# Kernel optimization log

Measured on AMD Instinct MI355X. Metric: run time of the kernel, lower is better.

Reference implementation:

```python
import jax, jax.numpy as jnp
from jax import lax
import numpy as np

K = 3
IMG = 512
BATCH = 32


def setup_inputs() -> dict:
    key = jax.random.key(0)
    k1, k2, k3 = jax.random.split(key, 3)
    x = jax.random.normal(k1, (BATCH, 1, IMG, IMG), dtype=jnp.float32)
    # Conv2d(1, K*K, K) weight/bias, torch default init scale ~ 1/sqrt(fan_in)
    fan_in = 1 * K * K
    bound = 1.0 / np.sqrt(fan_in)
    W = jax.random.uniform(k2, (K * K, 1, K, K), dtype=jnp.float32, minval=-bound, maxval=bound)
    b = jax.random.uniform(k3, (K * K,), dtype=jnp.float32, minval=-bound, maxval=bound)
    return {"x": x, "W": W, "b": b}


def reference(x, W, b):
    k = W.shape[-1]
    pad = k // 2                      # k_radius
    P = x.shape[-1] + k - 1           # padded/self.img_size spatial size
    # x_tmp = F.pad(x, pad on all sides); firstConv = Conv2d(1, k^2, k, padding=pad)(x_tmp)
    x_tmp = jnp.pad(x, ((0, 0), (0, 0), (pad, pad), (pad, pad)))
    fc = lax.conv_general_dilated(
        x_tmp, W, window_strides=(1, 1), padding=[(pad, pad), (pad, pad)],
        dimension_numbers=("NCHW", "OIHW", "NCHW"),
    ) + b[None, :, None, None]        # (B, k^2, P, P)
    t = jnp.tanh(fc)
    # F.pad(x, (k-1-i, i, k-1-j, j)) == xp[:, :, j:j+P, i:i+P] with xp padded by k-1 everywhere
    xp = jnp.pad(x, ((0, 0), (0, 0), (k - 1, k - 1), (k - 1, k - 1)))
    out = jnp.zeros((x.shape[0], 1, P, P), dtype=x.dtype)
    for i in range(k):                # small fixed k^2 loop over kernel taps
        for j in range(k):
            out = out + xp[:, :, j:j + P, i:i + P] * t[:, k * i + j][:, None]
    return out[:, :, pad:-pad, pad:-pad]
```

## Files before the change

### kernel.cpp

```cpp
#include <hip/hip_runtime.h>
#include <stdint.h>

#define IMG  512
#define CPT  8
#define CGRP (IMG / CPT)

typedef float    v2f   __attribute__((ext_vector_type(2)));
typedef _Float16 h2    __attribute__((ext_vector_type(2)));
typedef __fp16   f16x2 __attribute__((ext_vector_type(2)));

#define SCALE 2.8853900817779268f

static __device__ __forceinline__ h2 pkrtz(float a, float b) {
    f16x2 t = __builtin_amdgcn_cvt_pkrtz(a, b);
    return __builtin_bit_cast(h2, t);
}

#if __has_builtin(__builtin_amdgcn_fdot2)
#define FDOT2(a, b, c) __builtin_amdgcn_fdot2((a), (b), (c), false)
#else
static __device__ __forceinline__ float fdot2_sw(h2 a, h2 b, float c) {
    return fmaf((float)a.x, (float)b.x, fmaf((float)a.y, (float)b.y, c));
}
#define FDOT2(a, b, c) fdot2_sw((a), (b), (c))
#endif

__global__ void prepack_kernel(const float* __restrict__ W,
                               const float* __restrict__ B,
                               uint32_t* __restrict__ ws) {
    int c = threadIdx.x;
    if (c < 9) {
        const float* wc = W + c * 9;
#pragma unroll
        for (int k = 0; k < 4; ++k) {
            h2 t = pkrtz(wc[2 * k] * SCALE, wc[2 * k + 1] * SCALE);
            ws[c * 4 + k] = __builtin_bit_cast(uint32_t, t);
        }
        ((float*)ws)[36 + c] = wc[8] * SCALE;
        ((float*)ws)[45 + c] = B[c] * SCALE;
    }
}

__global__ __launch_bounds__(256) void fused_convtap_kernel(
    const float* __restrict__ x,
    const uint32_t* __restrict__ wsu,
    float* __restrict__ out)
{
    const float* w8v = (const float*)(wsu + 36);
    const float* bvv = (const float*)(wsu + 45);

    const int tid = blockIdx.x * 256 + threadIdx.x;
    const int xg  = tid & (CGRP - 1);
    const int row = tid >> 6;
    const int y   = row & (IMG - 1);
    const int x0  = xg * CPT;

    const float* xr = x + (size_t)row * IMG;

    h2 u[9][4];
#pragma unroll
    for (int c = 0; c < 9; ++c)
#pragma unroll
        for (int k = 0; k < 4; ++k)
            u[c][k] = __builtin_bit_cast(h2, wsu[c * 4 + k]);
    float w8[9], bv[9];
#pragma unroll
    for (int c = 0; c < 9; ++c) { w8[c] = w8v[c]; bv[c] = bvv[c]; }

    const bool has_l = (x0 > 0);
    const bool has_r = (x0 < IMG - CPT);

    float r0[10], r1[10], r2[10];
    auto load_row = [&](const float* p, float* r) {
        float4 a = *reinterpret_cast<const float4*>(p + x0);
        float4 c = *reinterpret_cast<const float4*>(p + x0 + 4);
        r[1] = a.x; r[2] = a.y; r[3] = a.z; r[4] = a.w;
        r[5] = c.x; r[6] = c.y; r[7] = c.z; r[8] = c.w;
        r[0] = has_l ? p[x0 - 1] : 0.0f;
        r[9] = has_r ? p[x0 + 8] : 0.0f;
    };
    auto zero_row = [&](float* r) {
#pragma unroll
        for (int k = 0; k < 10; ++k) r[k] = 0.0f;
    };

    if (y > 0)       load_row(xr - IMG, r0); else zero_row(r0);
                     load_row(xr,       r1);
    if (y < IMG - 1) load_row(xr + IMG, r2); else zero_row(r2);

    float o[CPT];
#pragma unroll
    for (int tp = 0; tp < 4; ++tp) {
        const int t0 = 2 * tp;
        h2 A0 = pkrtz(r0[t0],     r0[t0 + 1]);
        h2 B0 = pkrtz(r0[t0 + 2], r1[t0]);
        h2 C0 = pkrtz(r1[t0 + 1], r1[t0 + 2]);
        h2 D0 = pkrtz(r2[t0],     r2[t0 + 1]);
        h2 A1 = pkrtz(r0[t0 + 1], r0[t0 + 2]);
        h2 B1 = pkrtz(r0[t0 + 3], r1[t0 + 1]);
        h2 C1 = pkrtz(r1[t0 + 2], r1[t0 + 3]);
        h2 D1 = pkrtz(r2[t0 + 1], r2[t0 + 2]);

        v2f acc = {0.0f, 0.0f};
#pragma unroll
        for (int c = 0; c < 9; ++c) {
            float fx = bv[c], fy = bv[c];
            fx = FDOT2(A0, u[c][0], fx);
            fx = FDOT2(B0, u[c][1], fx);
            fx = FDOT2(C0, u[c][2], fx);
            fx = FDOT2(D0, u[c][3], fx);
            fx = fmaf(r2[t0 + 2], w8[c], fx);
            fy = FDOT2(A1, u[c][0], fy);
            fy = FDOT2(B1, u[c][1], fy);
            fy = FDOT2(C1, u[c][2], fy);
            fy = FDOT2(D1, u[c][3], fy);
            fy = fmaf(r2[t0 + 3], w8[c], fy);

            v2f e   = { __builtin_amdgcn_exp2f(fx), __builtin_amdgcn_exp2f(fy) };
            v2f ep1 = e + (v2f){1.0f, 1.0f};
            v2f rr  = { __builtin_amdgcn_rcpf(ep1.x), __builtin_amdgcn_rcpf(ep1.y) };
            v2f th  = __builtin_elementwise_fma((v2f){-2.0f, -2.0f}, rr,
                                                (v2f){1.0f, 1.0f});

            const int i = c / 3, j = c - 3 * i;
            const float* rj = (j == 0) ? r0 : (j == 1) ? r1 : r2;
            v2f px2 = { rj[t0 + i], rj[t0 + 1 + i] };
            acc = __builtin_elementwise_fma(px2, th, acc);
        }
        o[t0] = acc.x; o[t0 + 1] = acc.y;
    }

    float* orow = out + (size_t)row * IMG + x0;
    *reinterpret_cast<float4*>(orow)     = make_float4(o[0], o[1], o[2], o[3]);
    *reinterpret_cast<float4*>(orow + 4) = make_float4(o[4], o[5], o[6], o[7]);
}

extern "C" void kernel_launch(void* const* d_in, const int* in_sizes, int n_in,
                              void* d_out, int out_size, void* d_ws, size_t ws_size,
                              hipStream_t stream) {
    const float* x  = (const float*)d_in[0];
    const float* W  = (const float*)d_in[1];
    const float* Bv = (const float*)d_in[2];
    float* out = (float*)d_out;
    uint32_t* ws = (uint32_t*)d_ws;

    prepack_kernel<<<1, 64, 0, stream>>>(W, Bv, ws);

    const int batch   = in_sizes[0] / (IMG * IMG);
    const int threads = batch * IMG * CGRP;
    const int grid    = threads / 256;
    fused_convtap_kernel<<<grid, 256, 0, stream>>>(x, ws, out);
}
```

Before: 39.08 us.

## Replace tanh transcendentals with shared-memory lookup table and drop prepack kernel

Each block now builds a 4096-entry tanh table in LDS covering [-4,4] in steps of 1/512. The per-pixel exp2 and rcp evaluations become a clamped index computation and an LDS gather. The separate weight-prepacking kernel launch is removed: each thread now reads W and b directly and converts them to half pairs itself. This trades transcendental throughput for per-block table construction, a barrier, LDS bank-conflict risk, and a nearest-entry tanh approximation with small, input-independent error.

```diff
diff --git a/kernel.cpp b/kernel.cpp
--- a/kernel.cpp
+++ b/kernel.cpp
@@ -5,11 +5,8 @@
 #define CPT  8
 #define CGRP (IMG / CPT)
 
-typedef float    v2f   __attribute__((ext_vector_type(2)));
 typedef _Float16 h2    __attribute__((ext_vector_type(2)));
 typedef __fp16   f16x2 __attribute__((ext_vector_type(2)));
-
-#define SCALE 2.8853900817779268f
 
 static __device__ __forceinline__ h2 pkrtz(float a, float b) {
     f16x2 t = __builtin_amdgcn_cvt_pkrtz(a, b);
@@ -25,29 +22,22 @@
 #define FDOT2(a, b, c) fdot2_sw((a), (b), (c))
 #endif
 
-__global__ void prepack_kernel(const float* __restrict__ W,
-                               const float* __restrict__ B,
-                               uint32_t* __restrict__ ws) {
-    int c = threadIdx.x;
-    if (c < 9) {
-        const float* wc = W + c * 9;
-#pragma unroll
-        for (int k = 0; k < 4; ++k) {
-            h2 t = pkrtz(wc[2 * k] * SCALE, wc[2 * k + 1] * SCALE);
-            ws[c * 4 + k] = __builtin_bit_cast(uint32_t, t);
-        }
-        ((float*)ws)[36 + c] = wc[8] * SCALE;
-        ((float*)ws)[45 + c] = B[c] * SCALE;
-    }
-}
 
 __global__ __launch_bounds__(256) void fused_convtap_kernel(
     const float* __restrict__ x,
-    const uint32_t* __restrict__ wsu,
+    const float* __restrict__ W,
+    const float* __restrict__ Bv,
     float* __restrict__ out)
 {
-    const float* w8v = (const float*)(wsu + 36);
-    const float* bvv = (const float*)(wsu + 45);
+    __shared__ float lut[4096];
+#pragma unroll
+    for (int k = 0; k < 16; ++k) {
+        const int i  = threadIdx.x + (k << 8);
+        const float xi = fmaf((float)i, 0.001953125f, 0.0009765625f - 4.0f);
+        const float e  = __builtin_amdgcn_exp2f(xi * 2.8853900817779268f);
+        lut[i] = 1.0f - 2.0f * __builtin_amdgcn_rcpf(e + 1.0f);
+    }
+    __syncthreads();
 
     const int tid = blockIdx.x * 256 + threadIdx.x;
     const int xg  = tid & (CGRP - 1);
@@ -58,14 +48,15 @@
     const float* xr = x + (size_t)row * IMG;
 
     h2 u[9][4];
+    float w8[9], bv[9];
 #pragma unroll
-    for (int c = 0; c < 9; ++c)
+    for (int c = 0; c < 9; ++c) {
 #pragma unroll
         for (int k = 0; k < 4; ++k)
-            u[c][k] = __builtin_bit_cast(h2, wsu[c * 4 + k]);
-    float w8[9], bv[9];
-#pragma unroll
-    for (int c = 0; c < 9; ++c) { w8[c] = w8v[c]; bv[c] = bvv[c]; }
+            u[c][k] = pkrtz(W[c * 9 + 2 * k], W[c * 9 + 2 * k + 1]);
+        w8[c] = W[c * 9 + 8];
+        bv[c] = Bv[c];
+    }
 
     const bool has_l = (x0 > 0);
     const bool has_r = (x0 < IMG - CPT);
@@ -88,6 +79,12 @@
                      load_row(xr,       r1);
     if (y < IMG - 1) load_row(xr + IMG, r2); else zero_row(r2);
 
+    auto tlu = [&](float v) -> float {
+        float t = __builtin_amdgcn_fmed3f(fmaf(v, 512.0f, 2048.0f),
+                                          0.0f, 4095.0f);
+        return lut[(int)t];
+    };
+
     float o[CPT];
 #pragma unroll
     for (int tp = 0; tp < 4; ++tp) {
@@ -101,33 +98,30 @@
         h2 C1 = pkrtz(r1[t0 + 2], r1[t0 + 3]);
         h2 D1 = pkrtz(r2[t0 + 1], r2[t0 + 2]);
 
-        v2f acc = {0.0f, 0.0f};
+        float ox = 0.0f, oy = 0.0f;
 #pragma unroll
         for (int c = 0; c < 9; ++c) {
             float fx = bv[c], fy = bv[c];
             fx = FDOT2(A0, u[c][0], fx);
+            fy = FDOT2(A1, u[c][0], fy);
             fx = FDOT2(B0, u[c][1], fx);
+            fy = FDOT2(B1, u[c][1], fy);
             fx = FDOT2(C0, u[c][2], fx);
+            fy = FDOT2(C1, u[c][2], fy);
             fx = FDOT2(D0, u[c][3], fx);
+            fy = FDOT2(D1, u[c][3], fy);
             fx = fmaf(r2[t0 + 2], w8[c], fx);
-            fy = FDOT2(A1, u[c][0], fy);
-            fy = FDOT2(B1, u[c][1], fy);
-            fy = FDOT2(C1, u[c][2], fy);
-            fy = FDOT2(D1, u[c][3], fy);
             fy = fmaf(r2[t0 + 3], w8[c], fy);
 
-            v2f e   = { __builtin_amdgcn_exp2f(fx), __builtin_amdgcn_exp2f(fy) };
-            v2f ep1 = e + (v2f){1.0f, 1.0f};
-            v2f rr  = { __builtin_amdgcn_rcpf(ep1.x), __builtin_amdgcn_rcpf(ep1.y) };
-            v2f th  = __builtin_elementwise_fma((v2f){-2.0f, -2.0f}, rr,
-                                                (v2f){1.0f, 1.0f});
+            const float thx = tlu(fx);
+            const float thy = tlu(fy);
 
             const int i = c / 3, j = c - 3 * i;
             const float* rj = (j == 0) ? r0 : (j == 1) ? r1 : r2;
-            v2f px2 = { rj[t0 + i], rj[t0 + 1 + i] };
-            acc = __builtin_elementwise_fma(px2, th, acc);
+            ox = fmaf(rj[t0 + i],     thx, ox);
+            oy = fmaf(rj[t0 + 1 + i], thy, oy);
         }
-        o[t0] = acc.x; o[t0 + 1] = acc.y;
+        o[t0] = ox; o[t0 + 1] = oy;
     }
 
     float* orow = out + (size_t)row * IMG + x0;
@@ -142,12 +136,9 @@
     const float* W  = (const float*)d_in[1];
     const float* Bv = (const float*)d_in[2];
     float* out = (float*)d_out;
-    uint32_t* ws = (uint32_t*)d_ws;
-
-    prepack_kernel<<<1, 64, 0, stream>>>(W, Bv, ws);
 
     const int batch   = in_sizes[0] / (IMG * IMG);
     const int threads = batch * IMG * CGRP;
     const int grid    = threads / 256;
-    fused_convtap_kernel<<<grid, 256, 0, stream>>>(x, ws, out);
+    fused_convtap_kernel<<<grid, 256, 0, stream>>>(x, W, Bv, out);
 }
```

Result: slower. 40.28 us (+3.1%).
